# Kernel tuning notes

Measured on AMD Instinct MI355X. Metric: run time of the kernel, lower is better.

Reference implementation:

```python
import jax, jax.numpy as jnp
import numpy as np

L, D, H, FF, V, A, CTX, B, S = 6, 768, 12, 3072, 51865, 1500, 448, 32, 8
DH = D // H


def _ln(x, w, b, eps=1e-5):
    m = x.mean(-1, keepdims=True)
    v = ((x - m) ** 2).mean(-1, keepdims=True)
    return (x - m) * jax.lax.rsqrt(v + eps) * w + b


def _mha(q, k, v, mask=None):
    # q: [B,Sq,D], k/v: [B,T,D]
    b, sq, _ = q.shape
    t = k.shape[1]
    q = q.reshape(b, sq, H, DH)
    k = k.reshape(b, t, H, DH)
    v = v.reshape(b, t, H, DH)
    w = jnp.einsum('bsnd,btnd->bnst', q, k) * (DH ** -0.5)
    if mask is not None:
        w = w + mask
    w = jax.nn.softmax(w, axis=-1)
    return jnp.einsum('bnst,btnd->bsnd', w, v).reshape(b, sq, D)


def _forward(tokens, audio_features, token_emb, pos_emb, attn_ln_w, attn_ln_b,
             Wq, bq, Wk, Wv, bv, Wo, bo, cross_ln_w, cross_ln_b,
             cWq, cbq, cWk, cWv, cbv, cWo, cbo, mlp_ln_w, mlp_ln_b,
             W1, b1, W2, b2, ln_w, ln_b):
    s = tokens.shape[1]
    x = token_emb[tokens] + pos_emb[:s]  # [B,S,D]
    i_ = jnp.arange(s)
    mask = jnp.where(i_[None, :] > i_[:, None], -jnp.inf, 0.0).astype(x.dtype)
    for i in range(L):
        h = _ln(x, attn_ln_w[i], attn_ln_b[i])
        x = x + _mha(h @ Wq[i] + bq[i], h @ Wk[i], h @ Wv[i] + bv[i], mask) @ Wo[i] + bo[i]
        h = _ln(x, cross_ln_w[i], cross_ln_b[i])
        x = x + _mha(h @ cWq[i] + cbq[i], audio_features @ cWk[i],
                     audio_features @ cWv[i] + cbv[i]) @ cWo[i] + cbo[i]
        h = _ln(x, mlp_ln_w[i], mlp_ln_b[i])
        x = x + jax.nn.gelu(h @ W1[i] + b1[i], approximate=False) @ W2[i] + b2[i]
    x = _ln(x, ln_w, ln_b)
    return x @ token_emb.T  # [B,S,V]


def setup_inputs() -> dict:
    key = jax.random.key(0)
    ks = iter(jax.random.split(key, 40))
    def rn(shape, scale=0.02):
        return jax.random.normal(next(ks), shape, jnp.float32) * scale
    return {
        'tokens': jax.random.randint(next(ks), (B, S), 0, V),
        'audio_features': jax.random.normal(next(ks), (B, A, D), jnp.float32),
        'token_emb': rn((V, D)),
        'pos_emb': rn((CTX, D)),
        'attn_ln_w': jnp.ones((L, D)), 'attn_ln_b': jnp.zeros((L, D)),
        'Wq': rn((L, D, D)), 'bq': jnp.zeros((L, D)),
        'Wk': rn((L, D, D)),
        'Wv': rn((L, D, D)), 'bv': jnp.zeros((L, D)),
        'Wo': rn((L, D, D)), 'bo': jnp.zeros((L, D)),
        'cross_ln_w': jnp.ones((L, D)), 'cross_ln_b': jnp.zeros((L, D)),
        'cWq': rn((L, D, D)), 'cbq': jnp.zeros((L, D)),
        'cWk': rn((L, D, D)),
        'cWv': rn((L, D, D)), 'cbv': jnp.zeros((L, D)),
        'cWo': rn((L, D, D)), 'cbo': jnp.zeros((L, D)),
        'mlp_ln_w': jnp.ones((L, D)), 'mlp_ln_b': jnp.zeros((L, D)),
        'W1': rn((L, D, FF)), 'b1': jnp.zeros((L, FF)),
        'W2': rn((L, FF, D)), 'b2': jnp.zeros((L, D)),
        'ln_w': jnp.ones((D,)), 'ln_b': jnp.zeros((D,)),
    }


def reference(tokens, audio_features, token_emb, pos_emb, attn_ln_w, attn_ln_b,
              Wq, bq, Wk, Wv, bv, Wo, bo, cross_ln_w, cross_ln_b,
              cWq, cbq, cWk, cWv, cbv, cWo, cbo, mlp_ln_w, mlp_ln_b,
              W1, b1, W2, b2, ln_w, ln_b):
    return _forward(tokens, audio_features, token_emb, pos_emb, attn_ln_w, attn_ln_b,
                    Wq, bq, Wk, Wv, bv, Wo, bo, cross_ln_w, cross_ln_b,
                    cWq, cbq, cWk, cWv, cbv, cWo, cbo, mlp_ln_w, mlp_ln_b,
                    W1, b1, W2, b2, ln_w, ln_b)
```

## Files before the change

### kernel.cpp

```cpp
#include <hip/hip_runtime.h>
#include <hip/hip_bf16.h>

#define HH 12
#define DD 768
#define FFD 3072
#define AAn 1500
#define BBn 32
#define RR 256
#define VV 51865
#define VPAD2 52224
#define MAT (768*768)
#define LSTR ((size_t)8 * MAT + 2 * (size_t)DD * FFD)
#define TPAD 1536

#define OP_BIAS 1
#define OP_GELU 2
#define OP_RES  4
#define OP_BF16 8
#define OP_SCAT 16

typedef float f32x4 __attribute__((ext_vector_type(4)));
typedef short s16x8 __attribute__((ext_vector_type(8)));

__device__ __forceinline__ unsigned short f2bf(float f) {
  union { float f; unsigned int u; } v; v.f = f;
  unsigned int r = (v.u + 0x7fffu + ((v.u >> 16) & 1u)) >> 16;
  return (unsigned short)r;
}
__device__ __forceinline__ float bf2f_lo(unsigned int u) {
  union { unsigned int u; float f; } v; v.u = u << 16; return v.f;
}
__device__ __forceinline__ float bf2f_hi(unsigned int u) {
  union { unsigned int u; float f; } v; v.u = u & 0xffff0000u; return v.f;
}

__device__ __forceinline__ void gld_lds16(const unsigned short* g, unsigned short* l) {
  __builtin_amdgcn_global_load_lds(
      (const __attribute__((address_space(1))) void*)g,
      (__attribute__((address_space(3))) void*)l, 16, 0, 0);
}

__global__ void embed_k(const int* __restrict__ toks, const float* __restrict__ emb,
                        const float* __restrict__ pos, float* __restrict__ x) {
  int r = blockIdx.x;
  int s = r & 7;
  int t = toks[r];
  for (int c = threadIdx.x; c < DD; c += 256)
    x[(size_t)r * DD + c] = emb[(size_t)t * DD + c] + pos[(size_t)s * DD + c];
}

__global__ void cvt_bf16v(const float* __restrict__ src, unsigned short* __restrict__ dst,
                          long long n_src, long long n_tot) {
  long long g = ((long long)blockIdx.x * 256 + threadIdx.x) * 8;
  long long stride = (long long)gridDim.x * 256 * 8;
  for (; g < n_tot; g += stride) {
    union { unsigned short us[8]; s16x8 v; } pk;
    if (g + 8 <= n_src) {
      float4 f0 = *(const float4*)(src + g);
      float4 f1 = *(const float4*)(src + g + 4);
      pk.us[0] = f2bf(f0.x); pk.us[1] = f2bf(f0.y); pk.us[2] = f2bf(f0.z); pk.us[3] = f2bf(f0.w);
      pk.us[4] = f2bf(f1.x); pk.us[5] = f2bf(f1.y); pk.us[6] = f2bf(f1.z); pk.us[7] = f2bf(f1.w);
    } else {
      #pragma unroll
      for (int i = 0; i < 8; i++)
        pk.us[i] = (g + i < n_src) ? f2bf(src[g + i]) : (unsigned short)0;
    }
    *(s16x8*)(dst + g) = pk.v;
  }
}

__global__ void build_biases(const float* __restrict__ bq, const float* __restrict__ bv,
                             float* __restrict__ qkvb) {
  int i = blockIdx.x * 256 + threadIdx.x;
  if (i < 6 * 2304) {
    int l = i / 2304, n = i % 2304;
    qkvb[i] = (n < 768) ? bq[l * 768 + n] : (n < 1536 ? 0.f : bv[l * 768 + (n - 1536)]);
  }
}

__global__ __launch_bounds__(256) void ln_to_bf16(
    const float* __restrict__ x, const float* __restrict__ w,
    const float* __restrict__ b, unsigned short* __restrict__ out) {
  int row = blockIdx.x;
  const float* xr = x + (size_t)row * DD;
  int t = threadIdx.x;
  float v0 = xr[t], v1 = xr[t + 256], v2 = xr[t + 512];
  float s = v0 + v1 + v2;
  for (int o = 32; o; o >>= 1) s += __shfl_down(s, o);
  __shared__ float red[4], red2[4];
  int wid = t >> 6, lane = t & 63;
  if (!lane) red[wid] = s;
  __syncthreads();
  float mean = (red[0] + red[1] + red[2] + red[3]) * (1.f / DD);
  float d0 = v0 - mean, d1 = v1 - mean, d2 = v2 - mean;
  float s2 = d0 * d0 + d1 * d1 + d2 * d2;
  for (int o = 32; o; o >>= 1) s2 += __shfl_down(s2, o);
  if (!lane) red2[wid] = s2;
  __syncthreads();
  float var = (red2[0] + red2[1] + red2[2] + red2[3]) * (1.f / DD);
  float rstd = rsqrtf(var + 1e-5f);
  out[(size_t)row * DD + t]       = f2bf(d0 * rstd * w[t] + b[t]);
  out[(size_t)row * DD + t + 256] = f2bf(d1 * rstd * w[t + 256] + b[t + 256]);
  out[(size_t)row * DD + t + 512] = f2bf(d2 * rstd * w[t + 512] + b[t + 512]);
}

__global__ __launch_bounds__(256) void red_resid_ln(
    const float* __restrict__ part, int nparts, const float* __restrict__ bias,
    float* __restrict__ x, const float* __restrict__ w,
    const float* __restrict__ b, unsigned short* __restrict__ out) {
  int row = blockIdx.x;
  int t = threadIdx.x;
  float v[3];
  #pragma unroll
  for (int j = 0; j < 3; j++) {
    int c = t + j * 256;
    size_t i = (size_t)row * DD + c;
    float nv = x[i] + bias[c];
    for (int p = 0; p < nparts; p++) nv += part[(size_t)p * RR * DD + i];
    x[i] = nv;
    v[j] = nv;
  }
  float s = v[0] + v[1] + v[2];
  for (int o = 32; o; o >>= 1) s += __shfl_down(s, o);
  __shared__ float red[4], red2[4];
  int wid = t >> 6, lane = t & 63;
  if (!lane) red[wid] = s;
  __syncthreads();
  float mean = (red[0] + red[1] + red[2] + red[3]) * (1.f / DD);
  float d0 = v[0] - mean, d1 = v[1] - mean, d2 = v[2] - mean;
  float s2 = d0 * d0 + d1 * d1 + d2 * d2;
  for (int o = 32; o; o >>= 1) s2 += __shfl_down(s2, o);
  if (!lane) red2[wid] = s2;
  __syncthreads();
  float var = (red2[0] + red2[1] + red2[2] + red2[3]) * (1.f / DD);
  float rstd = rsqrtf(var + 1e-5f);
  out[(size_t)row * DD + t]       = f2bf(d0 * rstd * w[t] + b[t]);
  out[(size_t)row * DD + t + 256] = f2bf(d1 * rstd * w[t + 256] + b[t + 256]);
  out[(size_t)row * DD + t + 512] = f2bf(d2 * rstd * w[t + 512] + b[t + 512]);
}

struct WPtrs { const float* p[10]; };
__global__ __launch_bounds__(256) void transpose_w(
    WPtrs wp, unsigned short* __restrict__ dst) {
  int l = blockIdx.y;
  int idx = blockIdx.x;
  int zz, ct, rt, R, C;
  if (idx < 1152)      { zz = idx / 144; int t = idx % 144; ct = t % 12; rt = t / 12; R = DD; C = DD; }
  else if (idx < 1728) { zz = 8; int t = idx - 1152; ct = t % 48; rt = t / 48; R = DD; C = FFD; }
  else                 { zz = 9; int t = idx - 1728; rt = t % 48; ct = t / 48; R = FFD; C = DD; }
  const float* W = wp.p[zz] + (size_t)l * ((zz < 8) ? MAT : (size_t)DD * FFD);
  size_t doff = (zz < 8) ? (size_t)zz * MAT
                         : ((zz == 8) ? (size_t)8 * MAT : (size_t)8 * MAT + (size_t)FFD * DD);
  unsigned short* Wt = dst + (size_t)l * LSTR + doff;
  __shared__ unsigned short tile[64][65];
  int r0 = rt * 64, c0 = ct * 64;
  int tid = threadIdx.x;
  int rr = tid >> 3, cc = (tid & 7) * 8;
  #pragma unroll
  for (int j = 0; j < 2; j++) {
    int r = r0 + j * 32 + rr;
    const float* sp = W + (size_t)r * C + c0 + cc;
    float4 f0 = *(const float4*)sp, f1 = *(const float4*)(sp + 4);
    unsigned short* tp = &tile[j * 32 + rr][cc];
    tp[0] = f2bf(f0.x); tp[1] = f2bf(f0.y); tp[2] = f2bf(f0.z); tp[3] = f2bf(f0.w);
    tp[4] = f2bf(f1.x); tp[5] = f2bf(f1.y); tp[6] = f2bf(f1.z); tp[7] = f2bf(f1.w);
  }
  __syncthreads();
  #pragma unroll
  for (int j = 0; j < 2; j++) {
    int c = c0 + j * 32 + rr;
    union { unsigned short us[8]; s16x8 v; } pk;
    #pragma unroll
    for (int i = 0; i < 8; i++) pk.us[i] = tile[cc + i][j * 32 + rr];
    *(s16x8*)&Wt[(size_t)c * R + r0 + cc] = pk.v;
  }
}

__global__ __launch_bounds__(256) void audio_prep(
    const float* __restrict__ audio, unsigned short* __restrict__ a_bf,
    unsigned short* __restrict__ aT) {
  int b = blockIdx.z;
  int t0 = blockIdx.x * 64, e0 = blockIdx.y * 64;
  __shared__ unsigned short tile[64][65];
  int tid = threadIdx.x;
  const float* src = audio + (size_t)b * AAn * DD;
  unsigned short* dstb = a_bf + (size_t)b * AAn * DD;
  int rr = tid >> 3, cc = (tid & 7) * 8;
  #pragma unroll
  for (int j = 0; j < 2; j++) {
    int t = t0 + j * 32 + rr;
    union { unsigned short us[8]; s16x8 v; } pk;
    if (t < AAn) {
      const float* sp = src + (size_t)t * DD + e0 + cc;
      float4 f0 = *(const float4*)sp, f1 = *(const float4*)(sp + 4);
      pk.us[0] = f2bf(f0.x); pk.us[1] = f2bf(f0.y); pk.us[2] = f2bf(f0.z); pk.us[3] = f2bf(f0.w);
      pk.us[4] = f2bf(f1.x); pk.us[5] = f2bf(f1.y); pk.us[6] = f2bf(f1.z); pk.us[7] = f2bf(f1.w);
      *(s16x8*)&dstb[(size_t)t * DD + e0 + cc] = pk.v;
    } else {
      #pragma unroll
      for (int i = 0; i < 8; i++) pk.us[i] = 0;
    }
    unsigned short* tp = &tile[j * 32 + rr][cc];
    #pragma unroll
    for (int i = 0; i < 8; i++) tp[i] = pk.us[i];
  }
  __syncthreads();
  unsigned short* dstT = aT + (size_t)b * DD * TPAD;
  #pragma unroll
  for (int j = 0; j < 2; j++) {
    int e = e0 + j * 32 + rr;
    union { unsigned short us[8]; s16x8 v; } pk;
    #pragma unroll
    for (int i = 0; i < 8; i++) pk.us[i] = tile[cc + i][j * 32 + rr];
    *(s16x8*)&dstT[(size_t)e * TPAD + t0 + cc] = pk.v;
  }
}

template <int BM, int BN>
__global__ __launch_bounds__(256, 2) void gemm_t(
    const unsigned short* __restrict__ A, const unsigned short* __restrict__ Bt,
    void* __restrict__ Cv, const float* __restrict__ bias,
    const float* __restrict__ resid, int Klen, int Kstride, int Nout, int Cld,
    long zsA, long zsB, long zsC, long zsBias, int kz, int gmap, int op) {
  constexpr int WM = BM / 2, WN = BN / 2;
  constexpr int MREP = WM / 16, NREP = WN / 16;
  __shared__ unsigned short As[BM * 64];
  __shared__ unsigned short Bs[BN * 64];
  int bx = blockIdx.x, by = blockIdx.y, bz = blockIdx.z;
  if (gmap == 1) { int t = bx; bx = bz; bz = t; }
  else if (gmap == 2) {
    int id = bx;
    bx = (id >> 4) * 8 + (id & 7);
    by = (id >> 3) & 1;
    bz = 0;
  }
  const int n0 = bx * BN, m0 = by * BM;
  const int z = bz;
  const int kbeg = kz ? z * Klen : 0;
  const int tid = threadIdx.x, w = tid >> 6, l = tid & 63;
  const int wr = w >> 1, wc = w & 1;
  f32x4 acc[MREP][NREP] = {};

  const int rowA = l >> 3;
  const int colK = (l & 7) * 8;
  const unsigned short* gA =
      A + (size_t)z * zsA + (size_t)(m0 + w * (BM / 4) + rowA) * Kstride + colK + kbeg;
  const unsigned short* gB =
      Bt + (size_t)z * zsB + (size_t)(n0 + w * (BN / 4) + rowA) * Kstride + colK + kbeg;

  for (int k0 = 0; k0 < Klen; k0 += 64) {
    __syncthreads();
    #pragma unroll
    for (int p = 0; p < BM / 32; p++)
      gld_lds16(gA + (size_t)(p * 8) * Kstride + k0, &As[(w * (BM / 4) + p * 8) * 64]);
    #pragma unroll
    for (int p = 0; p < BN / 32; p++)
      gld_lds16(gB + (size_t)(p * 8) * Kstride + k0, &Bs[(w * (BN / 4) + p * 8) * 64]);
    __syncthreads();
    s16x8 aF[MREP][2], bF[NREP][2];
    #pragma unroll
    for (int m = 0; m < MREP; m++)
      #pragma unroll
      for (int kk = 0; kk < 2; kk++)
        aF[m][kk] = *(const s16x8*)&As[(wr * WM + m * 16 + (l & 15)) * 64 + kk * 32 + (l >> 4) * 8];
    #pragma unroll
    for (int n = 0; n < NREP; n++)
      #pragma unroll
      for (int kk = 0; kk < 2; kk++)
        bF[n][kk] = *(const s16x8*)&Bs[(wc * WN + n * 16 + (l & 15)) * 64 + kk * 32 + (l >> 4) * 8];
    #pragma unroll
    for (int m = 0; m < MREP; m++)
      #pragma unroll
      for (int n = 0; n < NREP; n++)
        #pragma unroll
        for (int kk = 0; kk < 2; kk++)
          acc[m][n] = __builtin_amdgcn_mfma_f32_16x16x32_bf16(aF[m][kk], bF[n][kk], acc[m][n], 0, 0, 0);
  }

  const float* biasz = (op & OP_BIAS) ? bias + (size_t)z * zsBias : nullptr;
  #pragma unroll
  for (int m = 0; m < MREP; m++) {
    int rr0 = m0 + wr * WM + m * 16 + (l >> 4) * 4;
    #pragma unroll
    for (int n = 0; n < NREP; n++) {
      int c = n0 + wc * WN + n * 16 + (l & 15);
      if (c < Nout) {
        float bval = (op & OP_BIAS) ? biasz[c] : 0.f;
        #pragma unroll
        for (int j = 0; j < 4; j++) {
          int r = rr0 + j;
          float val = acc[m][n][j] + bval;
          if (op & OP_GELU) val = 0.5f * val * (1.f + erff(val * 0.70710678118f));
          if (op & OP_RES)  val += resid[(size_t)r * Cld + c];
          if (op & OP_SCAT) {
            int hh = r >> 3;
            if (hh < HH)
              ((unsigned short*)Cv)[((size_t)hh * 256 + z * 8 + (r & 7)) * 768 + c] = f2bf(val);
          } else if (op & OP_BF16) {
            ((unsigned short*)Cv)[(size_t)z * zsC + (size_t)r * Cld + c] = f2bf(val);
          } else {
            ((float*)Cv)[(size_t)z * zsC + (size_t)r * Cld + c] = val;
          }
        }
      }
    }
  }
}

__global__ __launch_bounds__(64) void self_attn_k(
    const float* __restrict__ qkv, unsigned short* __restrict__ out) {
  int bh = blockIdx.x;
  int b = bh / HH, h = bh % HH;
  __shared__ float qs[8][65], ks[8][65], vs[8][65], ps[8][9];
  int l = threadIdx.x;
  for (int s = 0; s < 8; s++) {
    size_t base = ((size_t)(b * 8 + s)) * 2304 + h * 64 + l;
    qs[s][l] = qkv[base]; ks[s][l] = qkv[base + 768]; vs[s][l] = qkv[base + 1536];
  }
  __syncthreads();
  int s = l >> 3, t = l & 7;
  float sc = 0.f;
  #pragma unroll
  for (int d = 0; d < 64; d++) sc += qs[s][d] * ks[t][d];
  sc *= 0.125f;
  if (t > s) sc = -1e30f;
  float mx = sc;
  for (int o = 4; o; o >>= 1) mx = fmaxf(mx, __shfl_xor(mx, o, 8));
  float e = __expf(sc - mx);
  float sum = e;
  for (int o = 4; o; o >>= 1) sum += __shfl_xor(sum, o, 8);
  ps[s][t] = e / sum;
  __syncthreads();
  for (int s2 = 0; s2 < 8; s2++) {
    float acc = 0.f;
    #pragma unroll
    for (int t2 = 0; t2 < 8; t2++) acc += ps[s2][t2] * vs[t2][l];
    out[((size_t)(b * 8 + s2)) * DD + h * 64 + l] = f2bf(acc);
  }
}

__global__ __launch_bounds__(256) void qprime_k(
    const float* __restrict__ p2, const float* __restrict__ cbq,
    const float* __restrict__ cWk, unsigned short* __restrict__ Qp) {
  int bh = blockIdx.x;
  int b = bh / HH, h = bh % HH;
  __shared__ float qs[8][64];
  int tid = threadIdx.x;
  for (int i = tid; i < 512; i += 256) {
    int s = i >> 6, d = i & 63;
    size_t idx = (size_t)(b * 8 + s) * 768 + h * 64 + d;
    qs[s][d] = (p2[idx] + p2[(size_t)RR * DD + idx] + cbq[h * 64 + d]) * 0.125f;
  }
  __syncthreads();
  for (int e = tid; e < 768; e += 256) {
    const float* wr = cWk + (size_t)e * 768 + h * 64;
    float acc[8] = {};
    #pragma unroll 16
    for (int k = 0; k < 64; k++) {
      float wv = wr[k];
      #pragma unroll
      for (int s = 0; s < 8; s++) acc[s] += qs[s][k] * wv;
    }
    #pragma unroll
    for (int s = 0; s < 8; s++)
      Qp[((size_t)b * 128 + h * 8 + s) * 768 + e] = f2bf(acc[s]);
  }
}

__global__ __launch_bounds__(256) void xsoftmax_k(
    const unsigned short* __restrict__ S, unsigned short* __restrict__ P) {
  int bh = blockIdx.x;
  int b = bh / HH, h = bh % HH;
  int w = threadIdx.x >> 6, ln = threadIdx.x & 63;
  for (int rr = w; rr < 8; rr += 4) {
    size_t row = (size_t)b * 128 + h * 8 + rr;
    const unsigned int* sr = (const unsigned int*)(S + row * TPAD);
    unsigned int* pr = (unsigned int*)(P + row * TPAD);
    float v[24];
    float mx = -1e30f;
    #pragma unroll
    for (int i = 0; i < 12; i++) {
      unsigned int u = sr[ln + i * 64];
      int t0 = 2 * (ln + i * 64);
      v[2 * i]     = (t0 < AAn)     ? bf2f_lo(u) : -1e30f;
      v[2 * i + 1] = (t0 + 1 < AAn) ? bf2f_hi(u) : -1e30f;
      mx = fmaxf(mx, fmaxf(v[2 * i], v[2 * i + 1]));
    }
    for (int o = 32; o; o >>= 1) mx = fmaxf(mx, __shfl_xor(mx, o));
    float sum = 0.f;
    #pragma unroll
    for (int i = 0; i < 24; i++) { v[i] = __expf(v[i] - mx); sum += v[i]; }
    for (int o = 32; o; o >>= 1) sum += __shfl_xor(sum, o);
    float inv = 1.f / sum;
    #pragma unroll
    for (int i = 0; i < 12; i++) {
      int t0 = 2 * (ln + i * 64);
      unsigned int lo = (t0 < AAn)     ? f2bf(v[2 * i] * inv)     : 0;
      unsigned int hi = (t0 + 1 < AAn) ? f2bf(v[2 * i + 1] * inv) : 0;
      pr[ln + i * 64] = lo | (hi << 16);
    }
  }
}

static inline void* carve(char*& p, size_t bytes) {
  void* r = p;
  p += (bytes + 255) & ~(size_t)255;
  return r;
}

extern "C" void kernel_launch(void* const* d_in, const int* in_sizes, int n_in,
                              void* d_out, int out_size, void* d_ws, size_t ws_size,
                              hipStream_t stream) {
  const int*   tokens = (const int*)d_in[0];
  const float* audio  = (const float*)d_in[1];
  const float* temb   = (const float*)d_in[2];
  const float* pemb   = (const float*)d_in[3];
  const float* aln_w  = (const float*)d_in[4];
  const float* aln_b  = (const float*)d_in[5];
  const float* Wq = (const float*)d_in[6];
  const float* bq = (const float*)d_in[7];
  const float* Wk = (const float*)d_in[8];
  const float* Wv = (const float*)d_in[9];
  const float* bv = (const float*)d_in[10];
  const float* Wo = (const float*)d_in[11];
  const float* bo = (const float*)d_in[12];
  const float* cln_w = (const float*)d_in[13];
  const float* cln_b = (const float*)d_in[14];
  const float* cWq = (const float*)d_in[15];
  const float* cbq = (const float*)d_in[16];
  const float* cWk = (const float*)d_in[17];
  const float* cWv = (const float*)d_in[18];
  const float* cbv = (const float*)d_in[19];
  const float* cWo = (const float*)d_in[20];
  const float* cbo = (const float*)d_in[21];
  const float* mln_w = (const float*)d_in[22];
  const float* mln_b = (const float*)d_in[23];
  const float* W1 = (const float*)d_in[24];
  const float* b1 = (const float*)d_in[25];
  const float* W2 = (const float*)d_in[26];
  const float* b2 = (const float*)d_in[27];
  const float* lnw = (const float*)d_in[28];
  const float* lnb = (const float*)d_in[29];

  char* cur = (char*)d_ws;
  float* x    = (float*)carve(cur, (size_t)RR * DD * 4);
  float* qkv  = (float*)carve(cur, (size_t)RR * 2304 * 4);
  unsigned short* hb    = (unsigned short*)carve(cur, (size_t)RR * DD * 2);
  unsigned short* attnb = (unsigned short*)carve(cur, (size_t)RR * DD * 2);
  unsigned short* ffb   = (unsigned short*)carve(cur, (size_t)RR * FFD * 2);
  unsigned short* wt    = (unsigned short*)carve(cur, LSTR * 6 * 2);
  unsigned short* audio_bf = (unsigned short*)carve(cur, (size_t)BBn * AAn * DD * 2);
  unsigned short* audioT   = (unsigned short*)carve(cur, (size_t)BBn * DD * TPAD * 2);
  unsigned short* emb_bf = (unsigned short*)carve(cur, (size_t)VPAD2 * DD * 2);
  unsigned short* Sb = (unsigned short*)carve(cur, (size_t)BBn * 128 * TPAD * 2);
  unsigned short* Pb  = (unsigned short*)carve(cur, (size_t)BBn * 128 * TPAD * 2);
  unsigned short* Qp  = (unsigned short*)carve(cur, (size_t)BBn * 128 * DD * 2);
  unsigned short* Rbf = (unsigned short*)carve(cur, (size_t)HH * 256 * DD * 2);
  float* qkvb  = (float*)carve(cur, (size_t)6 * 2304 * 4);
  float* mlp2p = (float*)carve(cur, (size_t)4 * RR * DD * 4);

  auto G64 = [&](const unsigned short* A_, const unsigned short* Bt_, void* C_,
                 const float* bias_, const float* res_, int M_, int Np_,
                 int Klen_, int Kstr_, int Nout_, int Cld_, int op_,
                 int Z_ = 1, long zsA_ = 0, long zsB_ = 0, long zsC_ = 0,
                 long zsBias_ = 0, int kz_ = 0) {
    dim3 g(Np_ / 64, M_ / 64, Z_);
    gemm_t<64, 64><<<g, 256, 0, stream>>>(A_, Bt_, C_, bias_, res_,
        Klen_, Kstr_, Nout_, Cld_, zsA_, zsB_, zsC_, zsBias_, kz_, 0, op_);
  };

  embed_k<<<RR, 256, 0, stream>>>(tokens, temb, pemb, x);
  audio_prep<<<dim3(24, 12, BBn), 256, 0, stream>>>(audio, audio_bf, audioT);
  cvt_bf16v<<<4096, 256, 0, stream>>>(temb, emb_bf,
      (long long)VV * DD, (long long)VPAD2 * DD);
  build_biases<<<54, 256, 0, stream>>>(bq, bv, qkvb);

  WPtrs wp;
  wp.p[0] = Wq; wp.p[1] = Wk; wp.p[2] = Wv; wp.p[3] = Wo;
  wp.p[4] = cWq; wp.p[5] = cWk; wp.p[6] = cWv; wp.p[7] = cWo;
  wp.p[8] = W1; wp.p[9] = W2;
  transpose_w<<<dim3(2304, 6, 1), 256, 0, stream>>>(wp, wt);

  ln_to_bf16<<<RR, 256, 0, stream>>>(x, aln_w, aln_b, hb);

  for (int l = 0; l < 6; l++) {
    size_t vD = (size_t)l * DD;
    size_t vF = (size_t)l * FFD;
    unsigned short* wtl = wt + (size_t)l * LSTR;

    G64(hb, wtl, qkv, qkvb + (size_t)l * 2304, nullptr, RR, 2304, DD, DD, 2304, 2304, OP_BIAS);
    self_attn_k<<<BBn * HH, 64, 0, stream>>>(qkv, attnb);
    G64(attnb, wtl + (size_t)3 * MAT, mlp2p, nullptr, nullptr, RR, DD, 192, DD, DD, DD,
        0, 4, 0, 0, (long)RR * DD, 0, 1);
    red_resid_ln<<<RR, 256, 0, stream>>>(mlp2p, 4, bo + vD, x, cln_w + vD, cln_b + vD, hb);

    G64(hb, wtl + (size_t)4 * MAT, mlp2p, nullptr, nullptr, RR, DD, 384, DD, DD, DD,
        0, 2, 0, 0, (long)RR * DD, 0, 1);
    qprime_k<<<BBn * HH, 256, 0, stream>>>(mlp2p, cbq + vD, cWk + (size_t)l * MAT, Qp);
    {
      dim3 g(BBn, 1, TPAD / 64);
      gemm_t<128, 64><<<g, 256, 0, stream>>>(Qp, audio_bf, Sb, nullptr,
          nullptr, DD, DD, TPAD, TPAD, (long)128 * DD, (long)AAn * DD,
          (long)128 * TPAD, 0, 0, 1, OP_BF16);
    }
    xsoftmax_k<<<BBn * HH, 256, 0, stream>>>(Sb, Pb);
    {
      dim3 g(BBn, 1, DD / 32);
      gemm_t<128, 32><<<g, 256, 0, stream>>>(Pb, audioT, Rbf, nullptr,
          nullptr, TPAD, TPAD, DD, DD, (long)128 * TPAD, (long)DD * TPAD, 0, 0, 0, 1, OP_SCAT);
    }
    G64(Rbf, wtl + (size_t)6 * MAT, attnb, cbv + vD, nullptr, RR, 64, DD, DD, 64, DD,
        OP_BIAS | OP_BF16, HH, (long)256 * DD, (long)64 * DD, 64, 64, 0);
    G64(attnb, wtl + (size_t)7 * MAT, mlp2p, nullptr, nullptr, RR, DD, 192, DD, DD, DD,
        0, 4, 0, 0, (long)RR * DD, 0, 1);
    red_resid_ln<<<RR, 256, 0, stream>>>(mlp2p, 4, cbo + vD, x, mln_w + vD, mln_b + vD, hb);

    G64(hb, wtl + (size_t)8 * MAT, ffb, b1 + vF, nullptr, RR, FFD, DD, DD, FFD, FFD,
        OP_BIAS | OP_GELU | OP_BF16);
    G64(ffb, wtl + (size_t)8 * MAT + (size_t)DD * FFD, mlp2p, nullptr, nullptr,
        RR, DD, DD, FFD, DD, DD, 0, 4, 0, 0, (long)RR * DD, 0, 1);
    const float* nw = (l < 5) ? (aln_w + (size_t)(l + 1) * DD) : lnw;
    const float* nb = (l < 5) ? (aln_b + (size_t)(l + 1) * DD) : lnb;
    red_resid_ln<<<RR, 256, 0, stream>>>(mlp2p, 4, b2 + vD, x, nw, nb, hb);
  }

  {
    dim3 g(816, 1, 1);
    gemm_t<128, 128><<<g, 256, 0, stream>>>(hb, emb_bf, d_out, nullptr,
        nullptr, DD, DD, VV, VV, 0, 0, 0, 0, 0, 2, 0);
  }
}
```

Measured before the change: 1.350 ms.

## Use smaller GEMM tiles and deeper split-K to raise block counts

Several GEMMs switch to finer tiles: the QKV projection, the per-head value projection and the MLP up-projection use 32x32 tiles, and the vocab projection uses 64x128 tiles with a new block-index swizzle. Split-K depth goes from 4 to 6 for the attention output projections and from 2 to 6 for the cross-attention query projection, and the FF down-projection goes to 8 splits. The partial-sum buffer and the reduction kernels change to match. The MFMA inner loop now loads fragments per k-half, which lowers register pressure. The aim is more blocks in flight on the many CUs, at the cost of more partial-sum traffic and less operand reuse per tile.

Result: faster. 1.281 ms (-5.1%).

```diff
diff --git a/kernel.cpp b/kernel.cpp
--- a/kernel.cpp
+++ b/kernel.cpp
@@ -233,6 +233,11 @@
     bx = (id >> 4) * 8 + (id & 7);
     by = (id >> 3) & 1;
     bz = 0;
+  } else if (gmap == 3) {
+    int id = bx;
+    bx = ((id >> 5) << 3) | (id & 7);
+    by = (id >> 3) & 3;
+    bz = 0;
   }
   const int n0 = bx * BN, m0 = by * BM;
   const int z = bz;
@@ -257,24 +262,21 @@
     for (int p = 0; p < BN / 32; p++)
       gld_lds16(gB + (size_t)(p * 8) * Kstride + k0, &Bs[(w * (BN / 4) + p * 8) * 64]);
     __syncthreads();
-    s16x8 aF[MREP][2], bF[NREP][2];
-    #pragma unroll
-    for (int m = 0; m < MREP; m++)
+    #pragma unroll
+    for (int kk = 0; kk < 2; kk++) {
+      s16x8 aF[MREP], bF[NREP];
       #pragma unroll
-      for (int kk = 0; kk < 2; kk++)
-        aF[m][kk] = *(const s16x8*)&As[(wr * WM + m * 16 + (l & 15)) * 64 + kk * 32 + (l >> 4) * 8];
-    #pragma unroll
-    for (int n = 0; n < NREP; n++)
-      #pragma unroll
-      for (int kk = 0; kk < 2; kk++)
-        bF[n][kk] = *(const s16x8*)&Bs[(wc * WN + n * 16 + (l & 15)) * 64 + kk * 32 + (l >> 4) * 8];
-    #pragma unroll
-    for (int m = 0; m < MREP; m++)
+      for (int m = 0; m < MREP; m++)
+        aF[m] = *(const s16x8*)&As[(wr * WM + m * 16 + (l & 15)) * 64 + kk * 32 + (l >> 4) * 8];
       #pragma unroll
       for (int n = 0; n < NREP; n++)
+        bF[n] = *(const s16x8*)&Bs[(wc * WN + n * 16 + (l & 15)) * 64 + kk * 32 + (l >> 4) * 8];
+      #pragma unroll
+      for (int m = 0; m < MREP; m++)
         #pragma unroll
-        for (int kk = 0; kk < 2; kk++)
-          acc[m][n] = __builtin_amdgcn_mfma_f32_16x16x32_bf16(aF[m][kk], bF[n][kk], acc[m][n], 0, 0, 0);
+        for (int n = 0; n < NREP; n++)
+          acc[m][n] = __builtin_amdgcn_mfma_f32_16x16x32_bf16(aF[m], bF[n], acc[m][n], 0, 0, 0);
+    }
   }
 
   const float* biasz = (op & OP_BIAS) ? bias + (size_t)z * zsBias : nullptr;
@@ -349,7 +351,10 @@
   for (int i = tid; i < 512; i += 256) {
     int s = i >> 6, d = i & 63;
     size_t idx = (size_t)(b * 8 + s) * 768 + h * 64 + d;
-    qs[s][d] = (p2[idx] + p2[(size_t)RR * DD + idx] + cbq[h * 64 + d]) * 0.125f;
+    float acc = cbq[h * 64 + d];
+    #pragma unroll
+    for (int p = 0; p < 6; p++) acc += p2[(size_t)p * RR * DD + idx];
+    qs[s][d] = acc * 0.125f;
   }
   __syncthreads();
   for (int e = tid; e < 768; e += 256) {
@@ -457,7 +462,7 @@
   unsigned short* Qp  = (unsigned short*)carve(cur, (size_t)BBn * 128 * DD * 2);
   unsigned short* Rbf = (unsigned short*)carve(cur, (size_t)HH * 256 * DD * 2);
   float* qkvb  = (float*)carve(cur, (size_t)6 * 2304 * 4);
-  float* mlp2p = (float*)carve(cur, (size_t)4 * RR * DD * 4);
+  float* mlp2p = (float*)carve(cur, (size_t)8 * RR * DD * 4);
 
   auto G64 = [&](const unsigned short* A_, const unsigned short* Bt_, void* C_,
                  const float* bias_, const float* res_, int M_, int Np_,
@@ -468,6 +473,15 @@
     gemm_t<64, 64><<<g, 256, 0, stream>>>(A_, Bt_, C_, bias_, res_,
         Klen_, Kstr_, Nout_, Cld_, zsA_, zsB_, zsC_, zsBias_, kz_, 0, op_);
   };
+  auto G32 = [&](const unsigned short* A_, const unsigned short* Bt_, void* C_,
+                 const float* bias_, const float* res_, int M_, int Np_,
+                 int Klen_, int Kstr_, int Nout_, int Cld_, int op_,
+                 int Z_ = 1, long zsA_ = 0, long zsB_ = 0, long zsC_ = 0,
+                 long zsBias_ = 0, int kz_ = 0) {
+    dim3 g(Np_ / 32, M_ / 32, Z_);
+    gemm_t<32, 32><<<g, 256, 0, stream>>>(A_, Bt_, C_, bias_, res_,
+        Klen_, Kstr_, Nout_, Cld_, zsA_, zsB_, zsC_, zsBias_, kz_, 0, op_);
+  };
 
   embed_k<<<RR, 256, 0, stream>>>(tokens, temb, pemb, x);
   audio_prep<<<dim3(24, 12, BBn), 256, 0, stream>>>(audio, audio_bf, audioT);
@@ -488,14 +502,14 @@
     size_t vF = (size_t)l * FFD;
     unsigned short* wtl = wt + (size_t)l * LSTR;
 
-    G64(hb, wtl, qkv, qkvb + (size_t)l * 2304, nullptr, RR, 2304, DD, DD, 2304, 2304, OP_BIAS);
+    G32(hb, wtl, qkv, qkvb + (size_t)l * 2304, nullptr, RR, 2304, DD, DD, 2304, 2304, OP_BIAS);
     self_attn_k<<<BBn * HH, 64, 0, stream>>>(qkv, attnb);
-    G64(attnb, wtl + (size_t)3 * MAT, mlp2p, nullptr, nullptr, RR, DD, 192, DD, DD, DD,
-        0, 4, 0, 0, (long)RR * DD, 0, 1);
-    red_resid_ln<<<RR, 256, 0, stream>>>(mlp2p, 4, bo + vD, x, cln_w + vD, cln_b + vD, hb);
-
-    G64(hb, wtl + (size_t)4 * MAT, mlp2p, nullptr, nullptr, RR, DD, 384, DD, DD, DD,
-        0, 2, 0, 0, (long)RR * DD, 0, 1);
+    G64(attnb, wtl + (size_t)3 * MAT, mlp2p, nullptr, nullptr, RR, DD, 128, DD, DD, DD,
+        0, 6, 0, 0, (long)RR * DD, 0, 1);
+    red_resid_ln<<<RR, 256, 0, stream>>>(mlp2p, 6, bo + vD, x, cln_w + vD, cln_b + vD, hb);
+
+    G64(hb, wtl + (size_t)4 * MAT, mlp2p, nullptr, nullptr, RR, DD, 128, DD, DD, DD,
+        0, 6, 0, 0, (long)RR * DD, 0, 1);
     qprime_k<<<BBn * HH, 256, 0, stream>>>(mlp2p, cbq + vD, cWk + (size_t)l * MAT, Qp);
     {
       dim3 g(BBn, 1, TPAD / 64);
@@ -509,24 +523,24 @@
       gemm_t<128, 32><<<g, 256, 0, stream>>>(Pb, audioT, Rbf, nullptr,
           nullptr, TPAD, TPAD, DD, DD, (long)128 * TPAD, (long)DD * TPAD, 0, 0, 0, 1, OP_SCAT);
     }
-    G64(Rbf, wtl + (size_t)6 * MAT, attnb, cbv + vD, nullptr, RR, 64, DD, DD, 64, DD,
+    G32(Rbf, wtl + (size_t)6 * MAT, attnb, cbv + vD, nullptr, RR, 64, DD, DD, 64, DD,
         OP_BIAS | OP_BF16, HH, (long)256 * DD, (long)64 * DD, 64, 64, 0);
-    G64(attnb, wtl + (size_t)7 * MAT, mlp2p, nullptr, nullptr, RR, DD, 192, DD, DD, DD,
-        0, 4, 0, 0, (long)RR * DD, 0, 1);
-    red_resid_ln<<<RR, 256, 0, stream>>>(mlp2p, 4, cbo + vD, x, mln_w + vD, mln_b + vD, hb);
-
-    G64(hb, wtl + (size_t)8 * MAT, ffb, b1 + vF, nullptr, RR, FFD, DD, DD, FFD, FFD,
+    G64(attnb, wtl + (size_t)7 * MAT, mlp2p, nullptr, nullptr, RR, DD, 128, DD, DD, DD,
+        0, 6, 0, 0, (long)RR * DD, 0, 1);
+    red_resid_ln<<<RR, 256, 0, stream>>>(mlp2p, 6, cbo + vD, x, mln_w + vD, mln_b + vD, hb);
+
+    G32(hb, wtl + (size_t)8 * MAT, ffb, b1 + vF, nullptr, RR, FFD, DD, DD, FFD, FFD,
         OP_BIAS | OP_GELU | OP_BF16);
     G64(ffb, wtl + (size_t)8 * MAT + (size_t)DD * FFD, mlp2p, nullptr, nullptr,
-        RR, DD, DD, FFD, DD, DD, 0, 4, 0, 0, (long)RR * DD, 0, 1);
+        RR, DD, 384, FFD, DD, DD, 0, 8, 0, 0, (long)RR * DD, 0, 1);
     const float* nw = (l < 5) ? (aln_w + (size_t)(l + 1) * DD) : lnw;
     const float* nb = (l < 5) ? (aln_b + (size_t)(l + 1) * DD) : lnb;
-    red_resid_ln<<<RR, 256, 0, stream>>>(mlp2p, 4, b2 + vD, x, nw, nb, hb);
+    red_resid_ln<<<RR, 256, 0, stream>>>(mlp2p, 8, b2 + vD, x, nw, nb, hb);
   }
 
   {
-    dim3 g(816, 1, 1);
-    gemm_t<128, 128><<<g, 256, 0, stream>>>(hb, emb_bf, d_out, nullptr,
-        nullptr, DD, DD, VV, VV, 0, 0, 0, 0, 0, 2, 0);
-  }
-}
+    dim3 g(1632, 1, 1);
+    gemm_t<64, 128><<<g, 256, 0, stream>>>(hb, emb_bf, d_out, nullptr,
+        nullptr, DD, DD, VV, VV, 0, 0, 0, 0, 0, 3, 0);
+  }
+}
```
